# Optimization experiments

Measured on AMD Instinct MI355X. Metric: run time of the kernel, lower is better.

Reference implementation:

```python
import jax, jax.numpy as jnp
import numpy as np

D = 512          # hidden_dim
NH = 8           # num_heads
DH = D // NH     # head dim
N = 100000       # num_nodes
C = 64           # context size
E = 1600000      # num_edges (unused in math, required by signature)
LN_EPS = 1e-5


def layer_norm(x, g, b):
    mu = jnp.mean(x, axis=-1, keepdims=True)
    var = jnp.var(x, axis=-1, keepdims=True)
    return (x - mu) * jax.lax.rsqrt(var + LN_EPS) * g + b


def mha(q, kv, W_in, b_in, W_out, b_out):
    # torch nn.MultiheadAttention (batch of 1 folded out). q:[Lq,D], kv:[Lk,D]
    Wq, Wk, Wv = jnp.split(W_in, 3, axis=0)
    bq, bk, bv = jnp.split(b_in, 3)
    qh = (q @ Wq.T + bq).reshape(-1, NH, DH)
    kh = (kv @ Wk.T + bk).reshape(-1, NH, DH)
    vh = (kv @ Wv.T + bv).reshape(-1, NH, DH)
    scores = jnp.einsum('qhd,khd->hqk', qh, kh) * (DH ** -0.5)
    w = jax.nn.softmax(scores, axis=-1)
    out = jnp.einsum('hqk,khd->qhd', w, vh).reshape(-1, D)
    return out @ W_out.T + b_out


def setup_inputs() -> dict:
    key = jax.random.key(0)
    ks = jax.random.split(key, 12)
    s = 0.02
    return {
        'H': jax.random.normal(ks[0], (N, D), jnp.float32),
        'path_token': jax.random.normal(ks[1], (D,), jnp.float32),
        'W_in1': jax.random.normal(ks[2], (3 * D, D), jnp.float32) * s,
        'b_in1': jnp.zeros((3 * D,), jnp.float32),
        'W_out1': jax.random.normal(ks[3], (D, D), jnp.float32) * s,
        'b_out1': jnp.zeros((D,), jnp.float32),
        'W_in2': jax.random.normal(ks[4], (3 * D, D), jnp.float32) * s,
        'b_in2': jnp.zeros((3 * D,), jnp.float32),
        'W_out2': jax.random.normal(ks[5], (D, D), jnp.float32) * s,
        'b_out2': jnp.zeros((D,), jnp.float32),
        'ln1_g': jnp.ones((D,), jnp.float32),
        'ln1_b': jnp.zeros((D,), jnp.float32),
        'ln2_g': jnp.ones((D,), jnp.float32),
        'ln2_b': jnp.zeros((D,), jnp.float32),
        'edge_index': jax.random.randint(ks[6], (2, E), 0, N, jnp.int64)
            if jax.config.jax_enable_x64 else jax.random.randint(ks[6], (2, E), 0, N, jnp.int32),
        'context_ids': jax.random.randint(ks[7], (C,), 0, N, jnp.int32),
    }


def reference(H, path_token, W_in1, b_in1, W_out1, b_out1,
              W_in2, b_in2, W_out2, b_out2,
              ln1_g, ln1_b, ln2_g, ln2_b,
              edge_index, context_ids):
    # gather context node reprs [C, D]
    ctx = H[context_ids]
    # path attention: 1 query (path token) over C context keys/values
    upd = mha(path_token[None, :], ctx, W_in1, b_in1, W_out1, b_out1)[0]
    upd = layer_norm(upd + path_token, ln1_g, ln1_b)  # [D]
    # graph attention: every node queries N identical copies of `upd`.
    # All logits per query are equal -> softmax exactly uniform -> per-head
    # output == v_head(upd). So attn_out = out_proj(v_proj(upd)), identical
    # for every node (exact, not approximate).
    _, _, Wv2 = jnp.split(W_in2, 3, axis=0)
    bv2 = b_in2[2 * D:]
    v = upd @ Wv2.T + bv2                       # [D]
    attn2 = v @ W_out2.T + b_out2               # [D], broadcast over nodes
    H_cond = layer_norm(attn2[None, :] + H, ln2_g, ln2_b)  # [N, D]
    return H_cond
```

## Files before the change

kernel.cpp:

```cpp
#include <hip/hip_runtime.h>

#define D 512
#define NH 8
#define DH 64
#define CCTX 64
#define LN_EPS 1e-5f
#define NCHAIN 128

#define WS_T     0
#define WS_M     512
#define WS_CTX   5120
#define WS_CBAR  40960
#define WS_O     45056
#define WS_OUT1  45568
#define WS_V     46080
#define WS_ATTN2 46592
#define WS_FLAGS 47104

__device__ __forceinline__ float waveReduceSum(float v) {
#pragma unroll
    for (int off = 32; off > 0; off >>= 1) v += __shfl_xor(v, off);
    return v;
}

__device__ __forceinline__ void barFlags(unsigned* flags, unsigned phase) {
    __syncthreads();
    if (threadIdx.x == 0)
        __hip_atomic_store(&flags[blockIdx.x], phase, __ATOMIC_RELEASE,
                           __HIP_MEMORY_SCOPE_AGENT);
    if (threadIdx.x < 64) {
        while (true) {
            unsigned f0 = __hip_atomic_load(&flags[threadIdx.x],
                                            __ATOMIC_RELAXED, __HIP_MEMORY_SCOPE_AGENT);
            unsigned f1 = __hip_atomic_load(&flags[64 + threadIdx.x],
                                            __ATOMIC_RELAXED, __HIP_MEMORY_SCOPE_AGENT);
            if (__all(f0 >= phase && f1 >= phase)) break;
            __builtin_amdgcn_s_sleep(2);
        }
        __builtin_amdgcn_fence(__ATOMIC_ACQUIRE, "agent");
    }
    __syncthreads();
}

__global__ __launch_bounds__(128) void k_init(unsigned* flags) {
    flags[threadIdx.x] = 0u;
}

__device__ __forceinline__ void matvec_rows(
    const float* __restrict__ W, const float* __restrict__ x,
    const float* __restrict__ b, float* __restrict__ y, int headStride)
{
    int wib = threadIdx.x >> 6, lane = threadIdx.x & 63;
    int r = blockIdx.x * 4 + wib;
    const float* xr = x + (r >> 6) * headStride;
    const float* Wr = W + (size_t)r * D;
    float4 w0 = *(const float4*)(Wr + lane * 4);
    float4 w1 = *(const float4*)(Wr + 256 + lane * 4);
    float4 x0 = *(const float4*)(xr + lane * 4);
    float4 x1 = *(const float4*)(xr + 256 + lane * 4);
    float s = w0.x*x0.x + w0.y*x0.y + w0.z*x0.z + w0.w*x0.w
            + w1.x*x1.x + w1.y*x1.y + w1.z*x1.z + w1.w*x1.w;
    s = waveReduceSum(s);
    if (lane == 0) y[r] = s + b[r];
}

__global__ __launch_bounds__(256) void k_chain(
    const float* __restrict__ Hm,   const float* __restrict__ path,
    const float* __restrict__ Win1, const float* __restrict__ bin1,
    const float* __restrict__ Wout1,const float* __restrict__ bout1,
    const float* __restrict__ Win2, const float* __restrict__ bin2,
    const float* __restrict__ Wout2,const float* __restrict__ bout2,
    const float* __restrict__ ln1g, const float* __restrict__ ln1b,
    const int* __restrict__ ids,    float* __restrict__ ws)
{
    __shared__ __align__(16) float smem[532];
    unsigned* flags = (unsigned*)(ws + WS_FLAGS);
    const int B = blockIdx.x, tid = threadIdx.x;
    const int wib = tid >> 6, lane = tid & 63;

    if (B < 64) {
        if (tid < 128) {
            int id = ids[B];
            float4 v = *(const float4*)(Hm + (size_t)id * D + tid * 4);
            *(float4*)(ws + WS_CTX + B * D + tid * 4) = v;
        }
    } else if (B < 80) {
        int bm = B - 64;
        int h = bm >> 1, half = bm & 1;
        float* qh_lds = smem;
        {
            int r = tid >> 2, p = tid & 3;
            const float* wrow = Win1 + (size_t)(h * DH + r) * D + p * 128;
            const float* xrow = path + p * 128;
            float s = 0.f;
#pragma unroll 8
            for (int k = 0; k < 32; ++k) {
                float4 a = *(const float4*)(wrow + k * 4);
                float4 c = *(const float4*)(xrow + k * 4);
                s += a.x*c.x + a.y*c.y + a.z*c.z + a.w*c.w;
            }
            s += __shfl_xor(s, 1);
            s += __shfl_xor(s, 2);
            if (p == 0) qh_lds[r] = s + bin1[h * DH + r];
        }
        __syncthreads();
        {
            int c = half * 256 + tid;
            const float* Wk = Win1 + (size_t)D * D;
            float acc = 0.f;
#pragma unroll 8
            for (int d = 0; d < DH; ++d)
                acc += Wk[(size_t)(h * DH + d) * D + c] * qh_lds[d];
            ws[WS_M + h * D + c] = acc;
        }
        if (half == 0 && tid == 0) {
            float tt = 0.f;
            for (int d = 0; d < DH; ++d) tt += bin1[D + h * DH + d] * qh_lds[d];
            ws[WS_T + h] = tt;
        }
    }
    barFlags(flags, 1);

    if (B < NH) {
        const int h = B;
        float* s_lds = smem;
        float* w_lds = smem + 64;
        {
            int j = tid >> 2, p = tid & 3;
            const float* cr = ws + WS_CTX + j * D + p * 128;
            const float* mr = ws + WS_M + h * D + p * 128;
            float s = 0.f;
#pragma unroll 8
            for (int c4 = 0; c4 < 32; ++c4) {
                float4 a = *(const float4*)(cr + c4 * 4);
                float4 b = *(const float4*)(mr + c4 * 4);
                s += a.x*b.x + a.y*b.y + a.z*b.z + a.w*b.w;
            }
            s += __shfl_xor(s, 1);
            s += __shfl_xor(s, 2);
            if (p == 0) s_lds[j] = (s + ws[WS_T + h]) * 0.125f;
        }
        __syncthreads();
        if (wib == 0) {
            float sc = s_lds[lane];
            float mx = sc;
#pragma unroll
            for (int off = 32; off > 0; off >>= 1) mx = fmaxf(mx, __shfl_xor(mx, off));
            float e = __expf(sc - mx);
            float sum = waveReduceSum(e);
            w_lds[lane] = e / sum;
        }
        __syncthreads();
        for (int c = tid; c < D; c += 256) {
            float acc = 0.f;
#pragma unroll 8
            for (int j = 0; j < CCTX; ++j) acc += w_lds[j] * ws[WS_CTX + j * D + c];
            ws[WS_CBAR + h * D + c] = acc;
        }
    }
    barFlags(flags, 2);

    matvec_rows(Win1 + 2 * (size_t)D * D, ws + WS_CBAR, bin1 + 2 * D, ws + WS_O, D);
    barFlags(flags, 3);

    matvec_rows(Wout1, ws + WS_O, bout1, ws + WS_OUT1, 0);
    barFlags(flags, 4);

    {
        float* xs  = smem;
        float* red = smem + 520;
        float a0 = ws[WS_OUT1 + tid * 2]     + path[tid * 2];
        float a1 = ws[WS_OUT1 + tid * 2 + 1] + path[tid * 2 + 1];
        float s  = a0 + a1;
        float s2 = a0 * a0 + a1 * a1;
        s  = waveReduceSum(s);
        s2 = waveReduceSum(s2);
        if (lane == 0) { red[wib] = s; red[4 + wib] = s2; }
        __syncthreads();
        float st  = red[0] + red[1] + red[2] + red[3];
        float s2t = red[4] + red[5] + red[6] + red[7];
        float mu   = st * (1.f / D);
        float var  = s2t * (1.f / D) - mu * mu;
        float rinv = rsqrtf(var + LN_EPS);
        xs[tid * 2]     = (a0 - mu) * rinv * ln1g[tid * 2]     + ln1b[tid * 2];
        xs[tid * 2 + 1] = (a1 - mu) * rinv * ln1g[tid * 2 + 1] + ln1b[tid * 2 + 1];
        __syncthreads();
        matvec_rows(Win2 + 2 * (size_t)D * D, xs, bin2 + 2 * D, ws + WS_V, 0);
    }
    barFlags(flags, 5);

    matvec_rows(Wout2, ws + WS_V, bout2, ws + WS_ATTN2, 0);
}

__global__ __launch_bounds__(256) void k_final(
    const float* __restrict__ Hm, const float* __restrict__ attn2,
    const float* __restrict__ g, const float* __restrict__ b,
    float* __restrict__ out, int N)
{
    const int lane = threadIdx.x & 63;
    const int wib  = threadIdx.x >> 6;
    const int w    = blockIdx.x * 4 + wib;
    const int STRIDE = 16384;

    const int c0 = lane * 4, c1 = 256 + lane * 4;
    float4 a0 = *(const float4*)(attn2 + c0), a1 = *(const float4*)(attn2 + c1);
    float4 g0 = *(const float4*)(g + c0),     g1 = *(const float4*)(g + c1);
    float4 b0 = *(const float4*)(b + c0),     b1 = *(const float4*)(b + c1);

    const float4* H4 = (const float4*)Hm;
    float4*       O4 = (float4*)out;
    const float4  z4 = {0.f, 0.f, 0.f, 0.f};

    int base = w * 2;
    if (base >= N) return;

    size_t i0 = (size_t)base * 128 + lane;
    float4 xa0 = H4[i0], xa1 = H4[i0 + 64];
    bool hasB = (base + 1) < N;
    float4 xb0 = hasB ? H4[i0 + 128] : z4;
    float4 xb1 = hasB ? H4[i0 + 192] : z4;

    while (true) {
        int  nbase = base + STRIDE;
        bool more  = nbase < N;
        float4 na0, na1, nb0, nb1;
        bool nHasB = false;
        if (more) {
            size_t ii = (size_t)nbase * 128 + lane;
            na0 = H4[ii]; na1 = H4[ii + 64];
            nHasB = (nbase + 1) < N;
            nb0 = nHasB ? H4[ii + 128] : z4;
            nb1 = nHasB ? H4[ii + 192] : z4;
        }

        float4 pa0, pa1, pb0, pb1;
        pa0.x = xa0.x + a0.x; pa0.y = xa0.y + a0.y; pa0.z = xa0.z + a0.z; pa0.w = xa0.w + a0.w;
        pa1.x = xa1.x + a1.x; pa1.y = xa1.y + a1.y; pa1.z = xa1.z + a1.z; pa1.w = xa1.w + a1.w;
        pb0.x = xb0.x + a0.x; pb0.y = xb0.y + a0.y; pb0.z = xb0.z + a0.z; pb0.w = xb0.w + a0.w;
        pb1.x = xb1.x + a1.x; pb1.y = xb1.y + a1.y; pb1.z = xb1.z + a1.z; pb1.w = xb1.w + a1.w;

        float sA  = pa0.x + pa0.y + pa0.z + pa0.w + pa1.x + pa1.y + pa1.z + pa1.w;
        float s2A = pa0.x*pa0.x + pa0.y*pa0.y + pa0.z*pa0.z + pa0.w*pa0.w
                  + pa1.x*pa1.x + pa1.y*pa1.y + pa1.z*pa1.z + pa1.w*pa1.w;
        float sB  = pb0.x + pb0.y + pb0.z + pb0.w + pb1.x + pb1.y + pb1.z + pb1.w;
        float s2B = pb0.x*pb0.x + pb0.y*pb0.y + pb0.z*pb0.z + pb0.w*pb0.w
                  + pb1.x*pb1.x + pb1.y*pb1.y + pb1.z*pb1.z + pb1.w*pb1.w;

#pragma unroll
        for (int off = 32; off > 0; off >>= 1) {
            sA  += __shfl_xor(sA,  off);
            s2A += __shfl_xor(s2A, off);
            sB  += __shfl_xor(sB,  off);
            s2B += __shfl_xor(s2B, off);
        }

        float muA   = sA * (1.f / D);
        float varA  = s2A * (1.f / D) - muA * muA;
        float rinvA = rsqrtf(varA + LN_EPS);
        float muB   = sB * (1.f / D);
        float varB  = s2B * (1.f / D) - muB * muB;
        float rinvB = rsqrtf(varB + LN_EPS);

        float4 y;
        y.x = (pa0.x - muA) * rinvA * g0.x + b0.x;
        y.y = (pa0.y - muA) * rinvA * g0.y + b0.y;
        y.z = (pa0.z - muA) * rinvA * g0.z + b0.z;
        y.w = (pa0.w - muA) * rinvA * g0.w + b0.w;
        O4[i0] = y;
        y.x = (pa1.x - muA) * rinvA * g1.x + b1.x;
        y.y = (pa1.y - muA) * rinvA * g1.y + b1.y;
        y.z = (pa1.z - muA) * rinvA * g1.z + b1.z;
        y.w = (pa1.w - muA) * rinvA * g1.w + b1.w;
        O4[i0 + 64] = y;
        if (hasB) {
            y.x = (pb0.x - muB) * rinvB * g0.x + b0.x;
            y.y = (pb0.y - muB) * rinvB * g0.y + b0.y;
            y.z = (pb0.z - muB) * rinvB * g0.z + b0.z;
            y.w = (pb0.w - muB) * rinvB * g0.w + b0.w;
            O4[i0 + 128] = y;
            y.x = (pb1.x - muB) * rinvB * g1.x + b1.x;
            y.y = (pb1.y - muB) * rinvB * g1.y + b1.y;
            y.z = (pb1.z - muB) * rinvB * g1.z + b1.z;
            y.w = (pb1.w - muB) * rinvB * g1.w + b1.w;
            O4[i0 + 192] = y;
        }

        if (!more) break;
        base = nbase;
        i0   = (size_t)base * 128 + lane;
        xa0 = na0; xa1 = na1; xb0 = nb0; xb1 = nb1;
        hasB = nHasB;
    }
}

extern "C" void kernel_launch(void* const* d_in, const int* in_sizes, int n_in,
                              void* d_out, int out_size, void* d_ws, size_t ws_size,
                              hipStream_t stream)
{
    const float* Hm    = (const float*)d_in[0];
    const float* path  = (const float*)d_in[1];
    const float* Win1  = (const float*)d_in[2];
    const float* bin1  = (const float*)d_in[3];
    const float* Wout1 = (const float*)d_in[4];
    const float* bout1 = (const float*)d_in[5];
    const float* Win2  = (const float*)d_in[6];
    const float* bin2  = (const float*)d_in[7];
    const float* Wout2 = (const float*)d_in[8];
    const float* bout2 = (const float*)d_in[9];
    const float* ln1g  = (const float*)d_in[10];
    const float* ln1b  = (const float*)d_in[11];
    const float* ln2g  = (const float*)d_in[12];
    const float* ln2b  = (const float*)d_in[13];
    const int*   ids   = (const int*)d_in[15];

    float* ws  = (float*)d_ws;
    float* out = (float*)d_out;
    const int N = in_sizes[0] / D;

    k_init<<<1, 128, 0, stream>>>((unsigned*)(ws + WS_FLAGS));
    k_chain<<<NCHAIN, 256, 0, stream>>>(Hm, path, Win1, bin1, Wout1, bout1,
                                        Win2, bin2, Wout2, bout2, ln1g, ln1b,
                                        ids, ws);
    k_final<<<2048, 256, 0, stream>>>(Hm, ws + WS_ATTN2, ln2g, ln2b, out, N);
}
```

Before: 140.8 us.

## Fuse chain and final LayerNorm into one persistent kernel with H prefetch

Merges the serial attention chain and the per-node LayerNorm pass into a single 2048-block kernel. Non-chain blocks stream their H rows once to warm the cache while the 128 chain blocks compute attn2, then spin on a done flag before applying LayerNorm to a contiguous 49-row chunk. Output stores become nontemporal. This hides the chain latency behind the H read and removes a kernel launch. In exchange it relies on all 2048 blocks being co-resident so the spin-waits cannot deadlock, and it depends on cache retention of about 100 KB per block.

```diff
diff --git a/kernel.cpp b/kernel.cpp
--- a/kernel.cpp
+++ b/kernel.cpp
@@ -6,6 +6,8 @@
 #define CCTX 64
 #define LN_EPS 1e-5f
 #define NCHAIN 128
+#define NGRID  2048
+#define CHF    49
 
 #define WS_T     0
 #define WS_M     512
@@ -16,6 +18,8 @@
 #define WS_V     46080
 #define WS_ATTN2 46592
 #define WS_FLAGS 47104
+
+typedef float f4v __attribute__((ext_vector_type(4)));
 
 __device__ __forceinline__ float waveReduceSum(float v) {
 #pragma unroll
@@ -42,8 +46,8 @@
     __syncthreads();
 }
 
-__global__ __launch_bounds__(128) void k_init(unsigned* flags) {
-    flags[threadIdx.x] = 0u;
+__global__ __launch_bounds__(256) void k_init(unsigned* flags) {
+    if (threadIdx.x < 192) flags[threadIdx.x] = 0u;
 }
 
 __device__ __forceinline__ void matvec_rows(
@@ -64,232 +68,231 @@
     if (lane == 0) y[r] = s + b[r];
 }
 
-__global__ __launch_bounds__(256) void k_chain(
+__global__ __launch_bounds__(256) void k_fused(
     const float* __restrict__ Hm,   const float* __restrict__ path,
     const float* __restrict__ Win1, const float* __restrict__ bin1,
     const float* __restrict__ Wout1,const float* __restrict__ bout1,
     const float* __restrict__ Win2, const float* __restrict__ bin2,
     const float* __restrict__ Wout2,const float* __restrict__ bout2,
     const float* __restrict__ ln1g, const float* __restrict__ ln1b,
-    const int* __restrict__ ids,    float* __restrict__ ws)
+    const float* __restrict__ ln2g, const float* __restrict__ ln2b,
+    const int* __restrict__ ids,    float* __restrict__ ws,
+    float* __restrict__ out, int N)
 {
     __shared__ __align__(16) float smem[532];
     unsigned* flags = (unsigned*)(ws + WS_FLAGS);
+    unsigned* done  = flags + 160;
     const int B = blockIdx.x, tid = threadIdx.x;
     const int wib = tid >> 6, lane = tid & 63;
 
-    if (B < 64) {
-        if (tid < 128) {
-            int id = ids[B];
-            float4 v = *(const float4*)(Hm + (size_t)id * D + tid * 4);
-            *(float4*)(ws + WS_CTX + B * D + tid * 4) = v;
-        }
-    } else if (B < 80) {
-        int bm = B - 64;
-        int h = bm >> 1, half = bm & 1;
-        float* qh_lds = smem;
+    if (B >= NCHAIN) {
+        int s0r = B * CHF;
+        int e0r = s0r + CHF; if (e0r > N) e0r = N;
+        const float4* H4 = (const float4*)Hm;
+        float4 acc = {0.f, 0.f, 0.f, 0.f};
+        int lo = s0r * 128 + tid, hi = e0r * 128;
+#pragma unroll 4
+        for (int i = lo; i < hi; i += 256) {
+            float4 v = H4[i];
+            acc.x += v.x; acc.y += v.y; acc.z += v.z; acc.w += v.w;
+        }
+        asm volatile("" :: "v"(acc.x), "v"(acc.y), "v"(acc.z), "v"(acc.w));
+        if (tid == 0) {
+            while (__hip_atomic_load(done, __ATOMIC_RELAXED,
+                                     __HIP_MEMORY_SCOPE_AGENT) == 0u)
+                __builtin_amdgcn_s_sleep(127);
+        }
+        __syncthreads();
+        __builtin_amdgcn_fence(__ATOMIC_ACQUIRE, "agent");
+    } else {
+        if (B < 64) {
+            if (tid < 128) {
+                int id = ids[B];
+                float4 v = *(const float4*)(Hm + (size_t)id * D + tid * 4);
+                *(float4*)(ws + WS_CTX + B * D + tid * 4) = v;
+            }
+        } else if (B < 80) {
+            int bm = B - 64;
+            int h = bm >> 1, half = bm & 1;
+            float* qh_lds = smem;
+            {
+                int rr = tid >> 2, p = tid & 3;
+                const float* wrow = Win1 + (size_t)(h * DH + rr) * D + p * 128;
+                const float* xrow = path + p * 128;
+                float s = 0.f;
+#pragma unroll 8
+                for (int k = 0; k < 32; ++k) {
+                    float4 a = *(const float4*)(wrow + k * 4);
+                    float4 c = *(const float4*)(xrow + k * 4);
+                    s += a.x*c.x + a.y*c.y + a.z*c.z + a.w*c.w;
+                }
+                s += __shfl_xor(s, 1);
+                s += __shfl_xor(s, 2);
+                if (p == 0) qh_lds[rr] = s + bin1[h * DH + rr];
+            }
+            __syncthreads();
+            {
+                int c = half * 256 + tid;
+                const float* Wk = Win1 + (size_t)D * D;
+                float acc = 0.f;
+#pragma unroll 8
+                for (int d = 0; d < DH; ++d)
+                    acc += Wk[(size_t)(h * DH + d) * D + c] * qh_lds[d];
+                ws[WS_M + h * D + c] = acc;
+            }
+            if (half == 0 && tid == 0) {
+                float tt = 0.f;
+                for (int d = 0; d < DH; ++d) tt += bin1[D + h * DH + d] * qh_lds[d];
+                ws[WS_T + h] = tt;
+            }
+        }
+        barFlags(flags, 1);
+
+        if (B < NH) {
+            const int h = B;
+            float* s_lds = smem;
+            float* w_lds = smem + 64;
+            {
+                int j = tid >> 2, p = tid & 3;
+                const float* cr = ws + WS_CTX + j * D + p * 128;
+                const float* mr = ws + WS_M + h * D + p * 128;
+                float s = 0.f;
+#pragma unroll 8
+                for (int c4 = 0; c4 < 32; ++c4) {
+                    float4 a = *(const float4*)(cr + c4 * 4);
+                    float4 b = *(const float4*)(mr + c4 * 4);
+                    s += a.x*b.x + a.y*b.y + a.z*b.z + a.w*b.w;
+                }
+                s += __shfl_xor(s, 1);
+                s += __shfl_xor(s, 2);
+                if (p == 0) s_lds[j] = (s + ws[WS_T + h]) * 0.125f;
+            }
+            __syncthreads();
+            if (wib == 0) {
+                float sc = s_lds[lane];
+                float mx = sc;
+#pragma unroll
+                for (int off = 32; off > 0; off >>= 1) mx = fmaxf(mx, __shfl_xor(mx, off));
+                float e = __expf(sc - mx);
+                float sum = waveReduceSum(e);
+                w_lds[lane] = e / sum;
+            }
+            __syncthreads();
+            for (int c = tid; c < D; c += 256) {
+                float acc = 0.f;
+#pragma unroll 8
+                for (int j = 0; j < CCTX; ++j) acc += w_lds[j] * ws[WS_CTX + j * D + c];
+                ws[WS_CBAR + h * D + c] = acc;
+            }
+        }
+        barFlags(flags, 2);
+
+        matvec_rows(Win1 + 2 * (size_t)D * D, ws + WS_CBAR, bin1 + 2 * D, ws + WS_O, D);
+        barFlags(flags, 3);
+
+        matvec_rows(Wout1, ws + WS_O, bout1, ws + WS_OUT1, 0);
+        barFlags(flags, 4);
+
         {
-            int r = tid >> 2, p = tid & 3;
-            const float* wrow = Win1 + (size_t)(h * DH + r) * D + p * 128;
-            const float* xrow = path + p * 128;
-            float s = 0.f;
-#pragma unroll 8
-            for (int k = 0; k < 32; ++k) {
-                float4 a = *(const float4*)(wrow + k * 4);
-                float4 c = *(const float4*)(xrow + k * 4);
-                s += a.x*c.x + a.y*c.y + a.z*c.z + a.w*c.w;
-            }
-            s += __shfl_xor(s, 1);
-            s += __shfl_xor(s, 2);
-            if (p == 0) qh_lds[r] = s + bin1[h * DH + r];
-        }
-        __syncthreads();
-        {
-            int c = half * 256 + tid;
-            const float* Wk = Win1 + (size_t)D * D;
-            float acc = 0.f;
-#pragma unroll 8
-            for (int d = 0; d < DH; ++d)
-                acc += Wk[(size_t)(h * DH + d) * D + c] * qh_lds[d];
-            ws[WS_M + h * D + c] = acc;
-        }
-        if (half == 0 && tid == 0) {
-            float tt = 0.f;
-            for (int d = 0; d < DH; ++d) tt += bin1[D + h * DH + d] * qh_lds[d];
-            ws[WS_T + h] = tt;
-        }
+            float* xs  = smem;
+            float* red = smem + 520;
+            float a0 = ws[WS_OUT1 + tid * 2]     + path[tid * 2];
+            float a1 = ws[WS_OUT1 + tid * 2 + 1] + path[tid * 2 + 1];
+            float s  = a0 + a1;
+            float s2 = a0 * a0 + a1 * a1;
+            s  = waveReduceSum(s);
+            s2 = waveReduceSum(s2);
+            if (lane == 0) { red[wib] = s; red[4 + wib] = s2; }
+            __syncthreads();
+            float st  = red[0] + red[1] + red[2] + red[3];
+            float s2t = red[4] + red[5] + red[6] + red[7];
+            float mu   = st * (1.f / D);
+            float var  = s2t * (1.f / D) - mu * mu;
+            float rinv = rsqrtf(var + LN_EPS);
+            xs[tid * 2]     = (a0 - mu) * rinv * ln1g[tid * 2]     + ln1b[tid * 2];
+            xs[tid * 2 + 1] = (a1 - mu) * rinv * ln1g[tid * 2 + 1] + ln1b[tid * 2 + 1];
+            __syncthreads();
+            matvec_rows(Win2 + 2 * (size_t)D * D, xs, bin2 + 2 * D, ws + WS_V, 0);
+        }
+        barFlags(flags, 5);
+
+        matvec_rows(Wout2, ws + WS_V, bout2, ws + WS_ATTN2, 0);
+        barFlags(flags, 6);
+        if (tid == 0)
+            __hip_atomic_store(done, 1u, __ATOMIC_RELEASE, __HIP_MEMORY_SCOPE_AGENT);
     }
-    barFlags(flags, 1);
-
-    if (B < NH) {
-        const int h = B;
-        float* s_lds = smem;
-        float* w_lds = smem + 64;
-        {
-            int j = tid >> 2, p = tid & 3;
-            const float* cr = ws + WS_CTX + j * D + p * 128;
-            const float* mr = ws + WS_M + h * D + p * 128;
-            float s = 0.f;
-#pragma unroll 8
-            for (int c4 = 0; c4 < 32; ++c4) {
-                float4 a = *(const float4*)(cr + c4 * 4);
-                float4 b = *(const float4*)(mr + c4 * 4);
-                s += a.x*b.x + a.y*b.y + a.z*b.z + a.w*b.w;
-            }
-            s += __shfl_xor(s, 1);
-            s += __shfl_xor(s, 2);
-            if (p == 0) s_lds[j] = (s + ws[WS_T + h]) * 0.125f;
-        }
-        __syncthreads();
-        if (wib == 0) {
-            float sc = s_lds[lane];
-            float mx = sc;
+
+    {
+        const float* attn2 = ws + WS_ATTN2;
+        const int c0 = lane * 4, c1 = 256 + lane * 4;
+        float4 a0 = *(const float4*)(attn2 + c0), a1 = *(const float4*)(attn2 + c1);
+        float4 g0 = *(const float4*)(ln2g + c0),  g1 = *(const float4*)(ln2g + c1);
+        float4 b0 = *(const float4*)(ln2b + c0),  b1 = *(const float4*)(ln2b + c1);
+        const float4* H4 = (const float4*)Hm;
+        float4*       O4 = (float4*)out;
+        const float4  z4 = {0.f, 0.f, 0.f, 0.f};
+        int s0r = B * CHF;
+        int e0r = s0r + CHF; if (e0r > N) e0r = N;
+
+        for (int row = s0r + wib * 2; row < e0r; row += 8) {
+            bool hasB = (row + 1) < e0r;
+            size_t i0 = (size_t)row * 128 + lane;
+            float4 xa0 = H4[i0], xa1 = H4[i0 + 64];
+            float4 xb0 = hasB ? H4[i0 + 128] : z4;
+            float4 xb1 = hasB ? H4[i0 + 192] : z4;
+
+            float4 pa0, pa1, pb0, pb1;
+            pa0.x = xa0.x + a0.x; pa0.y = xa0.y + a0.y; pa0.z = xa0.z + a0.z; pa0.w = xa0.w + a0.w;
+            pa1.x = xa1.x + a1.x; pa1.y = xa1.y + a1.y; pa1.z = xa1.z + a1.z; pa1.w = xa1.w + a1.w;
+            pb0.x = xb0.x + a0.x; pb0.y = xb0.y + a0.y; pb0.z = xb0.z + a0.z; pb0.w = xb0.w + a0.w;
+            pb1.x = xb1.x + a1.x; pb1.y = xb1.y + a1.y; pb1.z = xb1.z + a1.z; pb1.w = xb1.w + a1.w;
+
+            float sA  = pa0.x + pa0.y + pa0.z + pa0.w + pa1.x + pa1.y + pa1.z + pa1.w;
+            float s2A = pa0.x*pa0.x + pa0.y*pa0.y + pa0.z*pa0.z + pa0.w*pa0.w
+                      + pa1.x*pa1.x + pa1.y*pa1.y + pa1.z*pa1.z + pa1.w*pa1.w;
+            float sB  = pb0.x + pb0.y + pb0.z + pb0.w + pb1.x + pb1.y + pb1.z + pb1.w;
+            float s2B = pb0.x*pb0.x + pb0.y*pb0.y + pb0.z*pb0.z + pb0.w*pb0.w
+                      + pb1.x*pb1.x + pb1.y*pb1.y + pb1.z*pb1.z + pb1.w*pb1.w;
+
 #pragma unroll
-            for (int off = 32; off > 0; off >>= 1) mx = fmaxf(mx, __shfl_xor(mx, off));
-            float e = __expf(sc - mx);
-            float sum = waveReduceSum(e);
-            w_lds[lane] = e / sum;
-        }
-        __syncthreads();
-        for (int c = tid; c < D; c += 256) {
-            float acc = 0.f;
-#pragma unroll 8
-            for (int j = 0; j < CCTX; ++j) acc += w_lds[j] * ws[WS_CTX + j * D + c];
-            ws[WS_CBAR + h * D + c] = acc;
-        }
-    }
-    barFlags(flags, 2);
-
-    matvec_rows(Win1 + 2 * (size_t)D * D, ws + WS_CBAR, bin1 + 2 * D, ws + WS_O, D);
-    barFlags(flags, 3);
-
-    matvec_rows(Wout1, ws + WS_O, bout1, ws + WS_OUT1, 0);
-    barFlags(flags, 4);
-
-    {
-        float* xs  = smem;
-        float* red = smem + 520;
-        float a0 = ws[WS_OUT1 + tid * 2]     + path[tid * 2];
-        float a1 = ws[WS_OUT1 + tid * 2 + 1] + path[tid * 2 + 1];
-        float s  = a0 + a1;
-        float s2 = a0 * a0 + a1 * a1;
-        s  = waveReduceSum(s);
-        s2 = waveReduceSum(s2);
-        if (lane == 0) { red[wib] = s; red[4 + wib] = s2; }
-        __syncthreads();
-        float st  = red[0] + red[1] + red[2] + red[3];
-        float s2t = red[4] + red[5] + red[6] + red[7];
-        float mu   = st * (1.f / D);
-        float var  = s2t * (1.f / D) - mu * mu;
-        float rinv = rsqrtf(var + LN_EPS);
-        xs[tid * 2]     = (a0 - mu) * rinv * ln1g[tid * 2]     + ln1b[tid * 2];
-        xs[tid * 2 + 1] = (a1 - mu) * rinv * ln1g[tid * 2 + 1] + ln1b[tid * 2 + 1];
-        __syncthreads();
-        matvec_rows(Win2 + 2 * (size_t)D * D, xs, bin2 + 2 * D, ws + WS_V, 0);
-    }
-    barFlags(flags, 5);
-
-    matvec_rows(Wout2, ws + WS_V, bout2, ws + WS_ATTN2, 0);
-}
-
-__global__ __launch_bounds__(256) void k_final(
-    const float* __restrict__ Hm, const float* __restrict__ attn2,
-    const float* __restrict__ g, const float* __restrict__ b,
-    float* __restrict__ out, int N)
-{
-    const int lane = threadIdx.x & 63;
-    const int wib  = threadIdx.x >> 6;
-    const int w    = blockIdx.x * 4 + wib;
-    const int STRIDE = 16384;
-
-    const int c0 = lane * 4, c1 = 256 + lane * 4;
-    float4 a0 = *(const float4*)(attn2 + c0), a1 = *(const float4*)(attn2 + c1);
-    float4 g0 = *(const float4*)(g + c0),     g1 = *(const float4*)(g + c1);
-    float4 b0 = *(const float4*)(b + c0),     b1 = *(const float4*)(b + c1);
-
-    const float4* H4 = (const float4*)Hm;
-    float4*       O4 = (float4*)out;
-    const float4  z4 = {0.f, 0.f, 0.f, 0.f};
-
-    int base = w * 2;
-    if (base >= N) return;
-
-    size_t i0 = (size_t)base * 128 + lane;
-    float4 xa0 = H4[i0], xa1 = H4[i0 + 64];
-    bool hasB = (base + 1) < N;
-    float4 xb0 = hasB ? H4[i0 + 128] : z4;
-    float4 xb1 = hasB ? H4[i0 + 192] : z4;
-
-    while (true) {
-        int  nbase = base + STRIDE;
-        bool more  = nbase < N;
-        float4 na0, na1, nb0, nb1;
-        bool nHasB = false;
-        if (more) {
-            size_t ii = (size_t)nbase * 128 + lane;
-            na0 = H4[ii]; na1 = H4[ii + 64];
-            nHasB = (nbase + 1) < N;
-            nb0 = nHasB ? H4[ii + 128] : z4;
-            nb1 = nHasB ? H4[ii + 192] : z4;
-        }
-
-        float4 pa0, pa1, pb0, pb1;
-        pa0.x = xa0.x + a0.x; pa0.y = xa0.y + a0.y; pa0.z = xa0.z + a0.z; pa0.w = xa0.w + a0.w;
-        pa1.x = xa1.x + a1.x; pa1.y = xa1.y + a1.y; pa1.z = xa1.z + a1.z; pa1.w = xa1.w + a1.w;
-        pb0.x = xb0.x + a0.x; pb0.y = xb0.y + a0.y; pb0.z = xb0.z + a0.z; pb0.w = xb0.w + a0.w;
-        pb1.x = xb1.x + a1.x; pb1.y = xb1.y + a1.y; pb1.z = xb1.z + a1.z; pb1.w = xb1.w + a1.w;
-
-        float sA  = pa0.x + pa0.y + pa0.z + pa0.w + pa1.x + pa1.y + pa1.z + pa1.w;
-        float s2A = pa0.x*pa0.x + pa0.y*pa0.y + pa0.z*pa0.z + pa0.w*pa0.w
-                  + pa1.x*pa1.x + pa1.y*pa1.y + pa1.z*pa1.z + pa1.w*pa1.w;
-        float sB  = pb0.x + pb0.y + pb0.z + pb0.w + pb1.x + pb1.y + pb1.z + pb1.w;
-        float s2B = pb0.x*pb0.x + pb0.y*pb0.y + pb0.z*pb0.z + pb0.w*pb0.w
-                  + pb1.x*pb1.x + pb1.y*pb1.y + pb1.z*pb1.z + pb1.w*pb1.w;
-
-#pragma unroll
-        for (int off = 32; off > 0; off >>= 1) {
-            sA  += __shfl_xor(sA,  off);
-            s2A += __shfl_xor(s2A, off);
-            sB  += __shfl_xor(sB,  off);
-            s2B += __shfl_xor(s2B, off);
-        }
-
-        float muA   = sA * (1.f / D);
-        float varA  = s2A * (1.f / D) - muA * muA;
-        float rinvA = rsqrtf(varA + LN_EPS);
-        float muB   = sB * (1.f / D);
-        float varB  = s2B * (1.f / D) - muB * muB;
-        float rinvB = rsqrtf(varB + LN_EPS);
-
-        float4 y;
-        y.x = (pa0.x - muA) * rinvA * g0.x + b0.x;
-        y.y = (pa0.y - muA) * rinvA * g0.y + b0.y;
-        y.z = (pa0.z - muA) * rinvA * g0.z + b0.z;
-        y.w = (pa0.w - muA) * rinvA * g0.w + b0.w;
-        O4[i0] = y;
-        y.x = (pa1.x - muA) * rinvA * g1.x + b1.x;
-        y.y = (pa1.y - muA) * rinvA * g1.y + b1.y;
-        y.z = (pa1.z - muA) * rinvA * g1.z + b1.z;
-        y.w = (pa1.w - muA) * rinvA * g1.w + b1.w;
-        O4[i0 + 64] = y;
-        if (hasB) {
-            y.x = (pb0.x - muB) * rinvB * g0.x + b0.x;
-            y.y = (pb0.y - muB) * rinvB * g0.y + b0.y;
-            y.z = (pb0.z - muB) * rinvB * g0.z + b0.z;
-            y.w = (pb0.w - muB) * rinvB * g0.w + b0.w;
-            O4[i0 + 128] = y;
-            y.x = (pb1.x - muB) * rinvB * g1.x + b1.x;
-            y.y = (pb1.y - muB) * rinvB * g1.y + b1.y;
-            y.z = (pb1.z - muB) * rinvB * g1.z + b1.z;
-            y.w = (pb1.w - muB) * rinvB * g1.w + b1.w;
-            O4[i0 + 192] = y;
-        }
-
-        if (!more) break;
-        base = nbase;
-        i0   = (size_t)base * 128 + lane;
-        xa0 = na0; xa1 = na1; xb0 = nb0; xb1 = nb1;
-        hasB = nHasB;
+            for (int off = 32; off > 0; off >>= 1) {
+                sA  += __shfl_xor(sA,  off);
+                s2A += __shfl_xor(s2A, off);
+                sB  += __shfl_xor(sB,  off);
+                s2B += __shfl_xor(s2B, off);
+            }
+
+            float muA   = sA * (1.f / D);
+            float varA  = s2A * (1.f / D) - muA * muA;
+            float rinvA = rsqrtf(varA + LN_EPS);
+            float muB   = sB * (1.f / D);
+            float varB  = s2B * (1.f / D) - muB * muB;
+            float rinvB = rsqrtf(varB + LN_EPS);
+
+            f4v y;
+            y.x = (pa0.x - muA) * rinvA * g0.x + b0.x;
+            y.y = (pa0.y - muA) * rinvA * g0.y + b0.y;
+            y.z = (pa0.z - muA) * rinvA * g0.z + b0.z;
+            y.w = (pa0.w - muA) * rinvA * g0.w + b0.w;
+            __builtin_nontemporal_store(y, (f4v*)(O4 + i0));
+            y.x = (pa1.x - muA) * rinvA * g1.x + b1.x;
+            y.y = (pa1.y - muA) * rinvA * g1.y + b1.y;
+            y.z = (pa1.z - muA) * rinvA * g1.z + b1.z;
+            y.w = (pa1.w - muA) * rinvA * g1.w + b1.w;
+            __builtin_nontemporal_store(y, (f4v*)(O4 + i0 + 64));
+            if (hasB) {
+                y.x = (pb0.x - muB) * rinvB * g0.x + b0.x;
+                y.y = (pb0.y - muB) * rinvB * g0.y + b0.y;
+                y.z = (pb0.z - muB) * rinvB * g0.z + b0.z;
+                y.w = (pb0.w - muB) * rinvB * g0.w + b0.w;
+                __builtin_nontemporal_store(y, (f4v*)(O4 + i0 + 128));
+                y.x = (pb1.x - muB) * rinvB * g1.x + b1.x;
+                y.y = (pb1.y - muB) * rinvB * g1.y + b1.y;
+                y.z = (pb1.z - muB) * rinvB * g1.z + b1.z;
+                y.w = (pb1.w - muB) * rinvB * g1.w + b1.w;
+                __builtin_nontemporal_store(y, (f4v*)(O4 + i0 + 192));
+            }
+        }
     }
 }
 
@@ -317,9 +320,8 @@
     float* out = (float*)d_out;
     const int N = in_sizes[0] / D;
 
-    k_init<<<1, 128, 0, stream>>>((unsigned*)(ws + WS_FLAGS));
-    k_chain<<<NCHAIN, 256, 0, stream>>>(Hm, path, Win1, bin1, Wout1, bout1,
-                                        Win2, bin2, Wout2, bout2, ln1g, ln1b,
-                                        ids, ws);
-    k_final<<<2048, 256, 0, stream>>>(Hm, ws + WS_ATTN2, ln2g, ln2b, out, N);
-}
+    k_init<<<1, 256, 0, stream>>>((unsigned*)(ws + WS_FLAGS));
+    k_fused<<<NGRID, 256, 0, stream>>>(Hm, path, Win1, bin1, Wout1, bout1,
+                                       Win2, bin2, Wout2, bout2, ln1g, ln1b,
+                                       ln2g, ln2b, ids, ws, out, N);
+}
```

Measured after the change: 190.3 us. 35.1% more time.
